# Performance work log

Measured on AMD Instinct MI355X. Metric: run time of the kernel, lower is better.

## Reference

```python
import jax, jax.numpy as jnp
import numpy as np

N = 100000      # num nodes
E = 1000000     # num directed edges
D_IN = 128      # input feature dim
D_H = 32        # hidden dim


def setup_inputs() -> dict:
    key = jax.random.key(0)
    ks = jax.random.split(key, 10)
    feat = jax.random.normal(ks[0], (N, D_IN), jnp.float32)
    src = jax.random.randint(ks[1], (E,), 0, N, dtype=jnp.int64)
    dst = jax.random.randint(ks[2], (E,), 0, N, dtype=jnp.int64)

    def lin(k, fan_in, fan_out):
        bound = 1.0 / np.sqrt(fan_in)
        kw, kb = jax.random.split(k)
        W = jax.random.uniform(kw, (fan_in, fan_out), jnp.float32, -bound, bound)
        b = jax.random.uniform(kb, (fan_out,), jnp.float32, -bound, bound)
        return W, b

    W_in, b_in = lin(ks[3], D_IN, D_H)        # input_project
    W_nbr, b_nbr = lin(ks[4], D_H, D_H)       # W_neighbor1 (Linear incl. its own bias)
    b_neighbor1 = jnp.zeros((D_H,), jnp.float32)  # extra learned bias, zero-init
    W_ffnn, b_ffnn = lin(ks[5], 2 * D_H, D_H)
    return {"feat": feat, "src": src, "dst": dst,
            "W_in": W_in, "b_in": b_in,
            "W_nbr": W_nbr, "b_nbr": b_nbr, "b_neighbor1": b_neighbor1,
            "W_ffnn": W_ffnn, "b_ffnn": b_ffnn}


def reference(feat, src, dst, W_in, b_in, W_nbr, b_nbr, b_neighbor1, W_ffnn, b_ffnn):
    # h = input_project(feat)  (input_dim != hidden_dim)
    h = feat @ W_in + b_in                                   # [N, D_H]

    # neighbors of v = predecessors (src where dst==v) + successors (dst where src==v)
    seg = jnp.concatenate([dst, src])                        # [2E] receiving node
    nbr = jnp.concatenate([src, dst])                        # [2E] neighbor node

    # sigmoid(W_neighbor1(h[nbr]) + b_neighbor1), then per-node max-pool
    t = jax.nn.sigmoid(h[nbr] @ W_nbr + b_nbr + b_neighbor1)  # [2E, D_H]
    agg = jax.ops.segment_max(t, seg, num_segments=N)         # [N, D_H]

    # nodes with total neighbor count <= 1 get zeros (faithful to `if len > 1`)
    deg = jax.ops.segment_sum(jnp.ones_like(seg, dtype=jnp.int32), seg, num_segments=N)
    agg = jnp.where((deg > 1)[:, None], agg, jnp.zeros((), jnp.float32))

    # concat + final linear
    out = jnp.concatenate([h, agg], axis=1) @ W_ffnn + b_ffnn  # [N, D_H]
    return out
```

## Files before the change

### kernel.cpp

```cpp
#include <hip/hip_runtime.h>
#include <hip/hip_bf16.h>

#define DH 32
#define BSZ 128
#define NBP 1024
#define SCAT_E 3840
#define SCAT_P (2 * SCAT_E)
#define EPT 15
#define PRE_E 8192
#define CPG 16
#define TS 4096
#define PAD 17
#define TPW 4

typedef short bf16x8 __attribute__((ext_vector_type(8)));
typedef float f32x4 __attribute__((ext_vector_type(4)));

__device__ __forceinline__ unsigned short f2bf(float x) {
    unsigned b = __float_as_uint(x);
    b += 0x7FFFu + ((b >> 16) & 1u);
    return (unsigned short)(b >> 16);
}

__global__ __launch_bounds__(256) void scan_buckets(
    const int* __restrict__ gtotal, int* __restrict__ gbase,
    int* __restrict__ gcursor)
{
    __shared__ int ss[256];
    const int t = threadIdx.x;
    int v0 = gtotal[4 * t], v1 = gtotal[4 * t + 1];
    int v2 = gtotal[4 * t + 2], v3 = gtotal[4 * t + 3];
    int tsum = v0 + v1 + v2 + v3;
    ss[t] = tsum;
    __syncthreads();
    for (int off = 1; off < 256; off <<= 1) {
        int y = (t >= off) ? ss[t - off] : 0;
        __syncthreads();
        ss[t] += y;
        __syncthreads();
    }
    int e = ss[t] - tsum;
    gbase[4 * t] = e;                    gcursor[4 * t] = e;
    gbase[4 * t + 1] = e + v0;           gcursor[4 * t + 1] = e + v0;
    gbase[4 * t + 2] = e + v0 + v1;      gcursor[4 * t + 2] = e + v0 + v1;
    gbase[4 * t + 3] = e + v0 + v1 + v2; gcursor[4 * t + 3] = e + v0 + v1 + v2;
}

__global__ __launch_bounds__(256) void precount_proj(
    const int* __restrict__ src, const int* __restrict__ dst,
    int* __restrict__ gtotal, int E, int jgrid,
    const float* __restrict__ feat,
    const float* __restrict__ W_in, const float* __restrict__ b_in,
    const float* __restrict__ W_nbr, const float* __restrict__ b_nbr,
    const float* __restrict__ b_n1,
    const float* __restrict__ W_ffnn, const float* __restrict__ b_ffnn,
    float* __restrict__ hpart, unsigned short* __restrict__ ub16,
    int N, int ntiles)
{
    __shared__ union {
        int hist[NBP];
        unsigned short htile[4][16 * 32];
    } sm;
    const int tid = threadIdx.x;

    if ((int)blockIdx.x >= jgrid) {
        for (int i = tid; i < NBP; i += 256) sm.hist[i] = 0;
        __syncthreads();
        const int e0 = ((int)blockIdx.x - jgrid) * PRE_E;
        const int eend = min(e0 + PRE_E, E);
        for (int e = e0 + tid; e < eend; e += 256) {
            atomicAdd(&sm.hist[src[e] >> 7], 1);
            atomicAdd(&sm.hist[dst[e] >> 7], 1);
        }
        __syncthreads();
        for (int i = tid; i < NBP; i += 256)
            if (sm.hist[i] > 0) atomicAdd(&gtotal[i], sm.hist[i]);
        return;
    }

    const int wid = tid >> 6, lane = tid & 63;
    const int r16 = lane & 15, kg = lane >> 4;

    bf16x8 B1[4][2], B2[2], Bf[2];
#pragma unroll
    for (int ks = 0; ks < 4; ++ks)
#pragma unroll
        for (int ct = 0; ct < 2; ++ct)
#pragma unroll
            for (int j = 0; j < 8; ++j)
                B1[ks][ct][j] = (short)f2bf(
                    W_in[(ks * 32 + kg * 8 + j) * 32 + ct * 16 + r16]);
#pragma unroll
    for (int ct = 0; ct < 2; ++ct)
#pragma unroll
        for (int j = 0; j < 8; ++j) {
            B2[ct][j] = (short)f2bf(W_nbr[(kg * 8 + j) * 32 + ct * 16 + r16]);
            Bf[ct][j] = (short)f2bf(W_ffnn[(kg * 8 + j) * 32 + ct * 16 + r16]);
        }

    const float b1a = b_in[r16],            b1b = b_in[16 + r16];
    const float b2a = b_nbr[r16] + b_n1[r16];
    const float b2b = b_nbr[16 + r16] + b_n1[16 + r16];
    const float bfa = b_ffnn[r16],          bfb = b_ffnn[16 + r16];

    unsigned short* hl = &sm.htile[wid][0];
    const int w = (int)blockIdx.x * 4 + wid;

    for (int i = 0; i < TPW; ++i) {
        const int t = w * TPW + i;
        if (t >= ntiles) break;
        const int tbase = t * 16;
        const int nA = tbase + r16;
        const bool okA = (nA < N);
        const float* fr = feat + (size_t)(okA ? nA : 0) * 128;

        bf16x8 A[4];
#pragma unroll
        for (int ks = 0; ks < 4; ++ks) {
            float4 p0 = make_float4(0.f, 0.f, 0.f, 0.f);
            float4 p1 = make_float4(0.f, 0.f, 0.f, 0.f);
            if (okA) {
                p0 = *(const float4*)(fr + ks * 32 + kg * 8);
                p1 = *(const float4*)(fr + ks * 32 + kg * 8 + 4);
            }
            A[ks][0] = (short)f2bf(p0.x); A[ks][1] = (short)f2bf(p0.y);
            A[ks][2] = (short)f2bf(p0.z); A[ks][3] = (short)f2bf(p0.w);
            A[ks][4] = (short)f2bf(p1.x); A[ks][5] = (short)f2bf(p1.y);
            A[ks][6] = (short)f2bf(p1.z); A[ks][7] = (short)f2bf(p1.w);
        }

        f32x4 acc0 = {b1a, b1a, b1a, b1a};
        f32x4 acc1 = {b1b, b1b, b1b, b1b};
#pragma unroll
        for (int ks = 0; ks < 4; ++ks) {
            acc0 = __builtin_amdgcn_mfma_f32_16x16x32_bf16(A[ks], B1[ks][0], acc0, 0, 0, 0);
            acc1 = __builtin_amdgcn_mfma_f32_16x16x32_bf16(A[ks], B1[ks][1], acc1, 0, 0, 0);
        }

#pragma unroll
        for (int r = 0; r < 4; ++r) {
            hl[(kg * 4 + r) * 32 + r16]      = f2bf(acc0[r]);
            hl[(kg * 4 + r) * 32 + 16 + r16] = f2bf(acc1[r]);
        }
        asm volatile("s_waitcnt lgkmcnt(0)" ::: "memory");
        bf16x8 A2 = *reinterpret_cast<const bf16x8*>(&hl[r16 * 32 + kg * 8]);

        f32x4 u0 = {b2a, b2a, b2a, b2a};
        f32x4 u1 = {b2b, b2b, b2b, b2b};
        u0 = __builtin_amdgcn_mfma_f32_16x16x32_bf16(A2, B2[0], u0, 0, 0, 0);
        u1 = __builtin_amdgcn_mfma_f32_16x16x32_bf16(A2, B2[1], u1, 0, 0, 0);
        f32x4 g0 = {bfa, bfa, bfa, bfa};
        f32x4 g1 = {bfb, bfb, bfb, bfb};
        g0 = __builtin_amdgcn_mfma_f32_16x16x32_bf16(A2, Bf[0], g0, 0, 0, 0);
        g1 = __builtin_amdgcn_mfma_f32_16x16x32_bf16(A2, Bf[1], g1, 0, 0, 0);

#pragma unroll
        for (int r = 0; r < 4; ++r) {
            const int n2 = tbase + kg * 4 + r;
            if (n2 < N) {
                float s0 = 1.0f / (1.0f + __expf(-u0[r]));
                float s1 = 1.0f / (1.0f + __expf(-u1[r]));
                ub16[(size_t)n2 * 16 + r16]              = f2bf(s0);
                ub16[((size_t)N + n2) * 16 + r16]        = f2bf(s1);
                hpart[(size_t)n2 * 32 + r16]      = g0[r];
                hpart[(size_t)n2 * 32 + 16 + r16] = g1[r];
            }
        }
    }
}

__global__ __launch_bounds__(256) void bucket_scatter(
    const int* __restrict__ src, const int* __restrict__ dst,
    int* __restrict__ gcursor, unsigned* __restrict__ pairs_g,
    int E, int B)
{
    __shared__ unsigned s_code[SCAT_P];
    __shared__ int s_cur[NBP];
    __shared__ int s_gbL[NBP];

    const int tid = threadIdx.x;
    const int e0 = blockIdx.x * SCAT_E;
    const int eend = min(e0 + SCAT_E, E);
    const int np = 2 * (eend - e0);

    for (int i = tid; i < NBP; i += 256) s_cur[i] = 0;
    __syncthreads();

    int es[EPT], dr[EPT];
#pragma unroll
    for (int j = 0; j < EPT; ++j) {
        int e = e0 + tid + j * 256;
        bool ok = (e < eend);
        es[j] = ok ? src[e] : -1;
        dr[j] = ok ? dst[e] : -1;
    }
#pragma unroll
    for (int j = 0; j < EPT; ++j) {
        if (es[j] >= 0) {
            atomicAdd(&s_cur[es[j] >> 7], 1);
            atomicAdd(&s_cur[dr[j] >> 7], 1);
        }
    }
    __syncthreads();

    {
        const int lane = tid & 63;
        const int w = tid >> 6;
        int v0 = s_cur[4 * tid], v1 = s_cur[4 * tid + 1];
        int v2 = s_cur[4 * tid + 2], v3 = s_cur[4 * tid + 3];
        int tsum = v0 + v1 + v2 + v3;
        int x = tsum;
#pragma unroll
        for (int off = 1; off < 64; off <<= 1) {
            int y = __shfl_up(x, off, 64);
            x += (lane >= off) ? y : 0;
        }
        if (lane == 63) s_gbL[w] = x;
        __syncthreads();
        int woff = 0;
#pragma unroll
        for (int k = 0; k < 4; ++k) woff += (k < w) ? s_gbL[k] : 0;
        int ebase = woff + x - tsum;
        __syncthreads();
        s_cur[4 * tid] = ebase;
        s_cur[4 * tid + 1] = ebase + v0;
        s_cur[4 * tid + 2] = ebase + v0 + v1;
        s_cur[4 * tid + 3] = ebase + v0 + v1 + v2;
    }
    __syncthreads();

#pragma unroll
    for (int j = 0; j < EPT; ++j) {
        if (es[j] >= 0) {
            int s = es[j], d = dr[j];
            int bs = s >> 7, bd = d >> 7;
            unsigned cs = ((unsigned)(bs & 255) << 24) |
                          ((unsigned)(s & 127) << 17) | (unsigned)d;
            unsigned cd = ((unsigned)(bd & 255) << 24) |
                          ((unsigned)(d & 127) << 17) | (unsigned)s;
            int p1 = atomicAdd(&s_cur[bs], 1);
            s_code[p1] = cs;
            int p2 = atomicAdd(&s_cur[bd], 1);
            s_code[p2] = cd;
        }
    }
    __syncthreads();

    for (int b = tid; b < B; b += 256) {
        int end = s_cur[b];
        int start = b ? s_cur[b - 1] : 0;
        int c = end - start;
        if (c > 0) {
            int gw = atomicAdd(&gcursor[b], c);
            s_gbL[b] = gw - start;
        }
    }
    __syncthreads();

    for (int i = tid; i < np; i += 256) {
        unsigned code = s_code[i];
        int cc = (int)(code >> 24);
#pragma unroll
        for (int k = 0; k < 3; ++k) {
            int hi2 = s_cur[cc];
            int lo2 = cc ? s_cur[cc - 1] : 0;
            bool in = (i < hi2) && (i >= lo2);
            cc = in ? cc : cc + 256;
        }
        pairs_g[s_gbL[cc] + i] = code & 0x00FFFFFFu;
    }
}

__global__ __launch_bounds__(256) void bucket_max(
    const unsigned* __restrict__ pairs_g, const int* __restrict__ gbase,
    const int* __restrict__ gtotal, const unsigned* __restrict__ ub32,
    float* __restrict__ agg, int N, int B)
{
    __shared__ unsigned aggL[BSZ * PAD];
    __shared__ int degL[BSZ];
    __shared__ unsigned tile[TS];

    const int tid = threadIdx.x;
    const int bid = blockIdx.x;
    const int xcd = bid & 7;
    const int q = xcd >> 2;
    const int b = (bid >> 3) * 4 + (xcd & 3);
    if (b >= B) return;
    const int v0 = b * BSZ;
    const unsigned* ut = ub32 + (size_t)q * N * 8;

    for (int i = tid; i < BSZ * PAD; i += 256) aggL[i] = 0u;
    for (int i = tid; i < BSZ; i += 256) degL[i] = 0;
    __syncthreads();

    const int start = gbase[b];
    const int cnt = gtotal[b];
    const int gg = tid >> 3;
    const int cl = tid & 7;

    for (int t0 = 0; t0 < cnt; t0 += TS) {
        const int tn = min(TS, cnt - t0);
        for (int i = tid; i < tn; i += 256) tile[i] = pairs_g[start + t0 + i];
        __syncthreads();

        const int kmax = (tn - gg + 31) >> 5;
        const int pm = tn - 1;
        for (int kk = 0; kk < kmax; kk += 16) {
            unsigned cc[16], xx[16];
#pragma unroll
            for (int u = 0; u < 16; ++u)
                cc[u] = tile[min(gg + (kk + u) * 32, pm)];
#pragma unroll
            for (int u = 0; u < 16; ++u)
                xx[u] = ut[(size_t)(cc[u] & 0x1FFFF) * 8 + cl];
#pragma unroll
            for (int u = 0; u < 16; ++u) {
                atomicMax(&aggL[(cc[u] >> 17) * PAD + 2 * cl], (xx[u] & 0xFFFFu) << 16);
                atomicMax(&aggL[(cc[u] >> 17) * PAD + 2 * cl + 1], xx[u] & 0xFFFF0000u);
            }
            if (cl == 0) {
#pragma unroll
                for (int u = 0; u < 16; ++u)
                    if (gg + (kk + u) * 32 < tn) atomicAdd(&degL[cc[u] >> 17], 1);
            }
        }
        __syncthreads();
    }

    for (int i = tid; i < BSZ * CPG; i += 256) {
        int vl = i >> 4;
        int v = v0 + vl;
        if (v < N) {
            float val = (degL[vl] > 1) ? __uint_as_float(aggL[vl * PAD + (i & 15)]) : 0.f;
            agg[(size_t)v * DH + q * CPG + (i & 15)] = val;
        }
    }
}

__global__ __launch_bounds__(256) void fin(
    const float* __restrict__ hpart, const float* __restrict__ agg,
    const float* __restrict__ W_ffnn, float* __restrict__ out, int N)
{
    const int node = blockIdx.x * 256 + threadIdx.x;
    if (node >= N) return;

    const float4* hr = (const float4*)(hpart + (size_t)node * 32);
    const float4* ar = (const float4*)(agg + (size_t)node * 32);

    float acc[32], a[32];
#pragma unroll
    for (int c4 = 0; c4 < 8; ++c4) {
        float4 v = hr[c4];
        acc[c4 * 4 + 0] = v.x; acc[c4 * 4 + 1] = v.y;
        acc[c4 * 4 + 2] = v.z; acc[c4 * 4 + 3] = v.w;
        float4 w = ar[c4];
        a[c4 * 4 + 0] = w.x; a[c4 * 4 + 1] = w.y;
        a[c4 * 4 + 2] = w.z; a[c4 * 4 + 3] = w.w;
    }

    const float* W2h = W_ffnn + 1024;
#pragma unroll
    for (int k = 0; k < 32; ++k) {
        const float hv = a[k];
        const float* wr = W2h + k * 32;
#pragma unroll
        for (int c = 0; c < 32; ++c)
            acc[c] = fmaf(hv, wr[c], acc[c]);
    }

    float4* orow = (float4*)(out + (size_t)node * 32);
#pragma unroll
    for (int c4 = 0; c4 < 8; ++c4)
        orow[c4] = make_float4(acc[c4 * 4 + 0], acc[c4 * 4 + 1],
                               acc[c4 * 4 + 2], acc[c4 * 4 + 3]);
}

extern "C" void kernel_launch(void* const* d_in, const int* in_sizes, int n_in,
                              void* d_out, int out_size, void* d_ws, size_t ws_size,
                              hipStream_t stream)
{
    const float* feat   = (const float*)d_in[0];
    const int*   src    = (const int*)d_in[1];
    const int*   dst    = (const int*)d_in[2];
    const float* W_in   = (const float*)d_in[3];
    const float* b_in   = (const float*)d_in[4];
    const float* W_nbr  = (const float*)d_in[5];
    const float* b_nbr  = (const float*)d_in[6];
    const float* b_n1   = (const float*)d_in[7];
    const float* W_ffnn = (const float*)d_in[8];
    const float* b_ffnn = (const float*)d_in[9];
    float* out = (float*)d_out;

    const int N = in_sizes[0] / 128;
    const int E = in_sizes[1];
    const int B = (N + BSZ - 1) / BSZ;
    const int ntiles = (N + 15) / 16;

    unsigned short* ub16 = (unsigned short*)out;
    float* hpart   = (float*)d_ws;
    float* agg     = hpart + (size_t)N * DH;
    int*   gtotal  = (int*)(agg + (size_t)N * DH);
    int*   gbase   = gtotal + NBP;
    int*   gcursor = gbase + NBP;
    unsigned* pairs_g = (unsigned*)(gcursor + NBP);

    const int egrid = (E + SCAT_E - 1) / SCAT_E;
    const int pgrid = (E + PRE_E - 1) / PRE_E;
    const int jgrid = (ntiles + 4 * TPW - 1) / (4 * TPW);
    const int npb = (N + 255) / 256;

    hipMemsetAsync(gtotal, 0, NBP * sizeof(int), stream);
    precount_proj<<<jgrid + pgrid, 256, 0, stream>>>(
        src, dst, gtotal, E, jgrid,
        feat, W_in, b_in, W_nbr, b_nbr, b_n1, W_ffnn, b_ffnn,
        hpart, ub16, N, ntiles);
    scan_buckets<<<1, 256, 0, stream>>>(gtotal, gbase, gcursor);
    bucket_scatter<<<egrid, 256, 0, stream>>>(src, dst, gcursor, pairs_g, E, B);
    bucket_max<<<((B + 3) / 4) * 8, 256, 0, stream>>>(
        pairs_g, gbase, gtotal, (const unsigned*)ub16, agg, N, B);
    fin<<<npb, 256, 0, stream>>>(hpart, agg, W_ffnn, out, N);
}
```

Measured before the change: 107.9 us.

## Pre-convert weights to transposed bf16 and give each wave one tile

A new single-block prep kernel zeroes the bucket histogram and converts W_in, W_nbr and W_ffnn once into transposed bf16 buffers in workspace, replacing the memset. The projection part of precount_proj now loads the weight fragments as vector bf16x8 reads instead of strided scalar float loads with per-element conversion. Each wave now handles one 16-row tile instead of four, so the grid is four times larger. This spreads the projection across more waves to hide latency, but each wave now pays the weight-load setup for only one tile, and an extra kernel launch is added.

```diff
diff --git a/kernel.cpp b/kernel.cpp
--- a/kernel.cpp
+++ b/kernel.cpp
@@ -11,7 +11,6 @@
 #define CPG 16
 #define TS 4096
 #define PAD 17
-#define TPW 4
 
 typedef short bf16x8 __attribute__((ext_vector_type(8)));
 typedef float f32x4 __attribute__((ext_vector_type(4)));
@@ -20,6 +19,24 @@
     unsigned b = __float_as_uint(x);
     b += 0x7FFFu + ((b >> 16) & 1u);
     return (unsigned short)(b >> 16);
+}
+
+__global__ __launch_bounds__(256) void prep(
+    const float* __restrict__ W_in, const float* __restrict__ W_nbr,
+    const float* __restrict__ W_ffnn,
+    unsigned short* __restrict__ wbf, int* __restrict__ gtotal)
+{
+    const int t = threadIdx.x;
+    for (int i = t; i < NBP; i += 256) gtotal[i] = 0;
+    for (int i = t; i < 4096; i += 256) {
+        int c = i >> 7, k = i & 127;
+        wbf[i] = f2bf(W_in[k * 32 + c]);
+    }
+    for (int i = t; i < 1024; i += 256) {
+        int c = i >> 5, k = i & 31;
+        wbf[4096 + i] = f2bf(W_nbr[k * 32 + c]);
+        wbf[5120 + i] = f2bf(W_ffnn[k * 32 + c]);
+    }
 }
 
 __global__ __launch_bounds__(256) void scan_buckets(
@@ -50,10 +67,9 @@
     const int* __restrict__ src, const int* __restrict__ dst,
     int* __restrict__ gtotal, int E, int jgrid,
     const float* __restrict__ feat,
-    const float* __restrict__ W_in, const float* __restrict__ b_in,
-    const float* __restrict__ W_nbr, const float* __restrict__ b_nbr,
-    const float* __restrict__ b_n1,
-    const float* __restrict__ W_ffnn, const float* __restrict__ b_ffnn,
+    const unsigned short* __restrict__ wbf,
+    const float* __restrict__ b_in, const float* __restrict__ b_nbr,
+    const float* __restrict__ b_n1, const float* __restrict__ b_ffnn,
     float* __restrict__ hpart, unsigned short* __restrict__ ub16,
     int N, int ntiles)
 {
@@ -80,91 +96,86 @@
 
     const int wid = tid >> 6, lane = tid & 63;
     const int r16 = lane & 15, kg = lane >> 4;
+    const int t = (int)blockIdx.x * 4 + wid;
+    if (t >= ntiles) return;
+
+    const unsigned short* W1t = wbf;
+    const unsigned short* W2t = wbf + 4096;
+    const unsigned short* Wft = wbf + 5120;
 
     bf16x8 B1[4][2], B2[2], Bf[2];
 #pragma unroll
     for (int ks = 0; ks < 4; ++ks)
 #pragma unroll
         for (int ct = 0; ct < 2; ++ct)
-#pragma unroll
-            for (int j = 0; j < 8; ++j)
-                B1[ks][ct][j] = (short)f2bf(
-                    W_in[(ks * 32 + kg * 8 + j) * 32 + ct * 16 + r16]);
-#pragma unroll
-    for (int ct = 0; ct < 2; ++ct)
-#pragma unroll
-        for (int j = 0; j < 8; ++j) {
-            B2[ct][j] = (short)f2bf(W_nbr[(kg * 8 + j) * 32 + ct * 16 + r16]);
-            Bf[ct][j] = (short)f2bf(W_ffnn[(kg * 8 + j) * 32 + ct * 16 + r16]);
-        }
+            B1[ks][ct] = *(const bf16x8*)&W1t[(ct * 16 + r16) * 128 + ks * 32 + kg * 8];
+#pragma unroll
+    for (int ct = 0; ct < 2; ++ct) {
+        B2[ct] = *(const bf16x8*)&W2t[(ct * 16 + r16) * 32 + kg * 8];
+        Bf[ct] = *(const bf16x8*)&Wft[(ct * 16 + r16) * 32 + kg * 8];
+    }
 
     const float b1a = b_in[r16],            b1b = b_in[16 + r16];
     const float b2a = b_nbr[r16] + b_n1[r16];
     const float b2b = b_nbr[16 + r16] + b_n1[16 + r16];
     const float bfa = b_ffnn[r16],          bfb = b_ffnn[16 + r16];
 
+    const int tbase = t * 16;
+    const int nA = tbase + r16;
+    const bool okA = (nA < N);
+    const float* fr = feat + (size_t)(okA ? nA : 0) * 128;
+
+    bf16x8 A[4];
+#pragma unroll
+    for (int ks = 0; ks < 4; ++ks) {
+        float4 p0 = make_float4(0.f, 0.f, 0.f, 0.f);
+        float4 p1 = make_float4(0.f, 0.f, 0.f, 0.f);
+        if (okA) {
+            p0 = *(const float4*)(fr + ks * 32 + kg * 8);
+            p1 = *(const float4*)(fr + ks * 32 + kg * 8 + 4);
+        }
+        A[ks][0] = (short)f2bf(p0.x); A[ks][1] = (short)f2bf(p0.y);
+        A[ks][2] = (short)f2bf(p0.z); A[ks][3] = (short)f2bf(p0.w);
+        A[ks][4] = (short)f2bf(p1.x); A[ks][5] = (short)f2bf(p1.y);
+        A[ks][6] = (short)f2bf(p1.z); A[ks][7] = (short)f2bf(p1.w);
+    }
+
+    f32x4 acc0 = {b1a, b1a, b1a, b1a};
+    f32x4 acc1 = {b1b, b1b, b1b, b1b};
+#pragma unroll
+    for (int ks = 0; ks < 4; ++ks) {
+        acc0 = __builtin_amdgcn_mfma_f32_16x16x32_bf16(A[ks], B1[ks][0], acc0, 0, 0, 0);
+        acc1 = __builtin_amdgcn_mfma_f32_16x16x32_bf16(A[ks], B1[ks][1], acc1, 0, 0, 0);
+    }
+
     unsigned short* hl = &sm.htile[wid][0];
-    const int w = (int)blockIdx.x * 4 + wid;
-
-    for (int i = 0; i < TPW; ++i) {
-        const int t = w * TPW + i;
-        if (t >= ntiles) break;
-        const int tbase = t * 16;
-        const int nA = tbase + r16;
-        const bool okA = (nA < N);
-        const float* fr = feat + (size_t)(okA ? nA : 0) * 128;
-
-        bf16x8 A[4];
-#pragma unroll
-        for (int ks = 0; ks < 4; ++ks) {
-            float4 p0 = make_float4(0.f, 0.f, 0.f, 0.f);
-            float4 p1 = make_float4(0.f, 0.f, 0.f, 0.f);
-            if (okA) {
-                p0 = *(const float4*)(fr + ks * 32 + kg * 8);
-                p1 = *(const float4*)(fr + ks * 32 + kg * 8 + 4);
-            }
-            A[ks][0] = (short)f2bf(p0.x); A[ks][1] = (short)f2bf(p0.y);
-            A[ks][2] = (short)f2bf(p0.z); A[ks][3] = (short)f2bf(p0.w);
-            A[ks][4] = (short)f2bf(p1.x); A[ks][5] = (short)f2bf(p1.y);
-            A[ks][6] = (short)f2bf(p1.z); A[ks][7] = (short)f2bf(p1.w);
-        }
-
-        f32x4 acc0 = {b1a, b1a, b1a, b1a};
-        f32x4 acc1 = {b1b, b1b, b1b, b1b};
-#pragma unroll
-        for (int ks = 0; ks < 4; ++ks) {
-            acc0 = __builtin_amdgcn_mfma_f32_16x16x32_bf16(A[ks], B1[ks][0], acc0, 0, 0, 0);
-            acc1 = __builtin_amdgcn_mfma_f32_16x16x32_bf16(A[ks], B1[ks][1], acc1, 0, 0, 0);
-        }
-
-#pragma unroll
-        for (int r = 0; r < 4; ++r) {
-            hl[(kg * 4 + r) * 32 + r16]      = f2bf(acc0[r]);
-            hl[(kg * 4 + r) * 32 + 16 + r16] = f2bf(acc1[r]);
-        }
-        asm volatile("s_waitcnt lgkmcnt(0)" ::: "memory");
-        bf16x8 A2 = *reinterpret_cast<const bf16x8*>(&hl[r16 * 32 + kg * 8]);
-
-        f32x4 u0 = {b2a, b2a, b2a, b2a};
-        f32x4 u1 = {b2b, b2b, b2b, b2b};
-        u0 = __builtin_amdgcn_mfma_f32_16x16x32_bf16(A2, B2[0], u0, 0, 0, 0);
-        u1 = __builtin_amdgcn_mfma_f32_16x16x32_bf16(A2, B2[1], u1, 0, 0, 0);
-        f32x4 g0 = {bfa, bfa, bfa, bfa};
-        f32x4 g1 = {bfb, bfb, bfb, bfb};
-        g0 = __builtin_amdgcn_mfma_f32_16x16x32_bf16(A2, Bf[0], g0, 0, 0, 0);
-        g1 = __builtin_amdgcn_mfma_f32_16x16x32_bf16(A2, Bf[1], g1, 0, 0, 0);
-
-#pragma unroll
-        for (int r = 0; r < 4; ++r) {
-            const int n2 = tbase + kg * 4 + r;
-            if (n2 < N) {
-                float s0 = 1.0f / (1.0f + __expf(-u0[r]));
-                float s1 = 1.0f / (1.0f + __expf(-u1[r]));
-                ub16[(size_t)n2 * 16 + r16]              = f2bf(s0);
-                ub16[((size_t)N + n2) * 16 + r16]        = f2bf(s1);
-                hpart[(size_t)n2 * 32 + r16]      = g0[r];
-                hpart[(size_t)n2 * 32 + 16 + r16] = g1[r];
-            }
+#pragma unroll
+    for (int r = 0; r < 4; ++r) {
+        hl[(kg * 4 + r) * 32 + r16]      = f2bf(acc0[r]);
+        hl[(kg * 4 + r) * 32 + 16 + r16] = f2bf(acc1[r]);
+    }
+    asm volatile("s_waitcnt lgkmcnt(0)" ::: "memory");
+    bf16x8 A2 = *reinterpret_cast<const bf16x8*>(&hl[r16 * 32 + kg * 8]);
+
+    f32x4 u0 = {b2a, b2a, b2a, b2a};
+    f32x4 u1 = {b2b, b2b, b2b, b2b};
+    u0 = __builtin_amdgcn_mfma_f32_16x16x32_bf16(A2, B2[0], u0, 0, 0, 0);
+    u1 = __builtin_amdgcn_mfma_f32_16x16x32_bf16(A2, B2[1], u1, 0, 0, 0);
+    f32x4 g0 = {bfa, bfa, bfa, bfa};
+    f32x4 g1 = {bfb, bfb, bfb, bfb};
+    g0 = __builtin_amdgcn_mfma_f32_16x16x32_bf16(A2, Bf[0], g0, 0, 0, 0);
+    g1 = __builtin_amdgcn_mfma_f32_16x16x32_bf16(A2, Bf[1], g1, 0, 0, 0);
+
+#pragma unroll
+    for (int r = 0; r < 4; ++r) {
+        const int n2 = tbase + kg * 4 + r;
+        if (n2 < N) {
+            float s0 = 1.0f / (1.0f + __expf(-u0[r]));
+            float s1 = 1.0f / (1.0f + __expf(-u1[r]));
+            ub16[(size_t)n2 * 16 + r16]       = f2bf(s0);
+            ub16[((size_t)N + n2) * 16 + r16] = f2bf(s1);
+            hpart[(size_t)n2 * 32 + r16]      = g0[r];
+            hpart[(size_t)n2 * 32 + 16 + r16] = g1[r];
         }
     }
 }
@@ -403,16 +414,17 @@
     int*   gbase   = gtotal + NBP;
     int*   gcursor = gbase + NBP;
     unsigned* pairs_g = (unsigned*)(gcursor + NBP);
+    unsigned short* wbf = (unsigned short*)(pairs_g + 2 * (size_t)E);
 
     const int egrid = (E + SCAT_E - 1) / SCAT_E;
     const int pgrid = (E + PRE_E - 1) / PRE_E;
-    const int jgrid = (ntiles + 4 * TPW - 1) / (4 * TPW);
+    const int jgrid = (ntiles + 3) / 4;
     const int npb = (N + 255) / 256;
 
-    hipMemsetAsync(gtotal, 0, NBP * sizeof(int), stream);
+    prep<<<1, 256, 0, stream>>>(W_in, W_nbr, W_ffnn, wbf, gtotal);
     precount_proj<<<jgrid + pgrid, 256, 0, stream>>>(
         src, dst, gtotal, E, jgrid,
-        feat, W_in, b_in, W_nbr, b_nbr, b_n1, W_ffnn, b_ffnn,
+        feat, wbf, b_in, b_nbr, b_n1, b_ffnn,
         hpart, ub16, N, ntiles);
     scan_buckets<<<1, 256, 0, stream>>>(gtotal, gbase, gcursor);
     bucket_scatter<<<egrid, 256, 0, stream>>>(src, dst, gcursor, pairs_g, E, B);
```

After: 114.9 us. +6.5%, slower.
